# Performance work log

Hardware: AMD Instinct MI355X
Metric: run time of the kernel (lower is better)

The kernel has to match this reference:

```python
import jax, jax.numpy as jnp
import numpy as np

B, T, H, E = 64, 48, 512, 512   # batch, max_length, hidden_size, embed_size (must equal H)
ATT, AF, FC, V = 196, 2048, 2048, 10000  # att_size, att_feat_size, fc_feat_size, vocab


def setup_inputs() -> dict:
    key = jax.random.key(0)
    ks = jax.random.split(key, 26)
    stdv = 1.0 / np.sqrt(H)

    def u(k, shape):
        return jax.random.uniform(k, shape, jnp.float32, -stdv, stdv)

    return {
        "word_idx": jax.random.randint(ks[0], (B, T), 0, V),
        "father_idx": jax.random.randint(ks[1], (B, T), 0, T),
        "fc_feats": jax.random.normal(ks[2], (B, FC), jnp.float32),
        "att_feats": jax.random.normal(ks[3], (B, ATT, AF), jnp.float32),
        # fc_embed / att_embed / word embedding
        "W_fc": u(ks[4], (E, FC)), "b_fc": u(ks[5], (E,)),
        "W_att": u(ks[6], (E, AF)), "b_att": u(ks[7], (E,)),
        "embed_tab": u(ks[8], (V, E)),
        # MDLSTMCell parameters
        "weight_f1": u(ks[9], (H, E + H)), "bias_f1": u(ks[10], (H,)),
        "weight_f2": u(ks[11], (H, E + H)), "bias_f2": u(ks[12], (H,)),
        "weight_H": u(ks[13], (2 * H, 2 * E + 2 * H)), "bias_H": u(ks[14], (2 * H,)),
        "weight_I": u(ks[15], (H, 2 * E + 2 * H + AF)), "bias_I": u(ks[16], (H,)),
        # attention core
        "W_ha": u(ks[17], (H, H)), "b_ha": u(ks[18], (H,)),
        "W_hf": u(ks[19], (H, H)), "b_hf": u(ks[20], (H,)),
        "W_alpha": u(ks[21], (1, H)), "b_alpha": u(ks[22], (1,)),
        # output logit
        "W_logit": u(ks[23], (V, H)), "b_logit": u(ks[24], (V,)),
    }


def _forward(word_idx, father_idx, fc_feats, att_feats,
             W_fc, b_fc, W_att, b_att, embed_tab,
             weight_f1, bias_f1, weight_f2, bias_f2,
             weight_H, bias_H, weight_I, bias_I,
             W_ha, b_ha, W_hf, b_hf, W_alpha, b_alpha,
             W_logit, b_logit):
    Bn, Tn = word_idx.shape
    Hd = weight_f1.shape[0]

    fc_emb = fc_feats @ W_fc.T + b_fc                 # [B, E]
    p_att = att_feats @ W_att.T + b_att               # [B, ATT, H]
    att_mean = att_feats.mean(axis=1)                 # [B, AF]
    barange = jnp.arange(Bn)

    def attention(ha, hf):
        # dot: [B, ATT, H]
        dot = jnp.tanh((ha @ W_ha.T + b_ha)[:, None, :]
                       + (hf @ W_hf.T + b_hf)[:, None, :] + p_att)
        logits = (dot @ W_alpha.T + b_alpha)[..., 0]  # [B, ATT]
        w = jax.nn.softmax(logits, axis=1)
        return jnp.einsum('ba,bad->bd', w, att_feats)  # [B, AF]

    def cell(x1, x2, h1, c1, h2, c2, att_res):
        cat = jnp.concatenate([x1, x2, h1, h2], axis=1)
        gates = cat @ weight_H.T + bias_H
        ingate, outgate = jnp.split(gates, 2, axis=1)
        ingate = jax.nn.sigmoid(ingate)
        outgate = jax.nn.sigmoid(outgate)
        cat_hat = jnp.concatenate([x1, x2, h1, h2, att_res], axis=1)
        cellgate = jnp.tanh(cat_hat @ weight_I.T + bias_I)
        f1 = jax.nn.sigmoid(jnp.concatenate([x1, h1], axis=1) @ weight_f1.T + bias_f1)
        f2 = jax.nn.sigmoid(jnp.concatenate([x2, h2], axis=1) @ weight_f2.T + bias_f2)
        nc = f1 * c1 + f2 * c2 + ingate * cellgate
        nh = outgate * jnp.tanh(nc)
        return nh, nc

    def step(carry, i):
        h_states, c_states = carry                    # each [B, T, H]
        father = father_idx[:, i]
        is_first = (i == 0)
        # ancestor branch (gathered from father position)
        w_a = word_idx[barange, father]
        x_a = jnp.where(is_first, fc_emb, embed_tab[w_a])
        h_a = jnp.where(is_first, 0.0, h_states[barange, father])
        c_a = jnp.where(is_first, 0.0, c_states[barange, father])
        # sibling branch (previous timestep, reset when (i-1) % 3 == 0)
        ip = jnp.maximum(i - 1, 0)
        use_f = jnp.logical_not(is_first | (((i - 1) % 3) == 0))
        x_f = jnp.where(use_f, embed_tab[word_idx[:, ip]], 0.0)
        h_f = jnp.where(use_f, h_states[:, ip], 0.0)
        c_f = jnp.where(use_f, c_states[:, ip], 0.0)
        att_res = jnp.where(is_first, att_mean, attention(h_a, h_f))
        nh, nc = cell(x_a, x_f, h_a, c_a, h_f, c_f, att_res)
        h_states = jax.lax.dynamic_update_slice(h_states, nh[:, None, :], (0, i, 0))
        c_states = jax.lax.dynamic_update_slice(c_states, nc[:, None, :], (0, i, 0))
        return (h_states, c_states), nh

    init = (jnp.zeros((Bn, Tn, Hd), jnp.float32), jnp.zeros((Bn, Tn, Hd), jnp.float32))
    _, outs = jax.lax.scan(step, init, jnp.arange(Tn))
    outs = jnp.transpose(outs, (1, 0, 2))             # [B, T, H]
    logits = outs @ W_logit.T + b_logit               # [B, T, V]
    return jax.nn.log_softmax(logits, axis=2)


def reference(word_idx, father_idx, fc_feats, att_feats,
              W_fc, b_fc, W_att, b_att, embed_tab,
              weight_f1, bias_f1, weight_f2, bias_f2,
              weight_H, bias_H, weight_I, bias_I,
              W_ha, b_ha, W_hf, b_hf, W_alpha, b_alpha,
              W_logit, b_logit):
    return _forward(word_idx, father_idx, fc_feats, att_feats,
                    W_fc, b_fc, W_att, b_att, embed_tab,
                    weight_f1, bias_f1, weight_f2, bias_f2,
                    weight_H, bias_H, weight_I, bias_I,
                    W_ha, b_ha, W_hf, b_hf, W_alpha, b_alpha,
                    W_logit, b_logit)
```

## Files before the change

kernel.cpp:

```cpp
#include <hip/hip_runtime.h>
#include <hip/hip_bf16.h>
#include <type_traits>

#define B_   64
#define T_   48
#define H_   512
#define E_   512
#define ATT_ 196
#define AF_  2048
#define FC_  2048
#define V_   10000

typedef unsigned short u16;
using s16x8 = __attribute__((ext_vector_type(8))) short;
using f32x4 = __attribute__((ext_vector_type(4))) float;

#define MD_BF16 0
#define MD_F32  1
#define MD_DYN  2

__device__ __forceinline__ float b2f(u16 u) {
  union { unsigned int i; float f; } x; x.i = ((unsigned int)u) << 16; return x.f;
}
__device__ __forceinline__ u16 f2b(float f) {
  union { float f; unsigned int i; } x; x.f = f;
  unsigned int r = x.i + 0x7fffu + ((x.i >> 16) & 1u);
  return (u16)(r >> 16);
}
__device__ __forceinline__ float sigmoid_(float x) { return 1.f / (1.f + __expf(-x)); }
__device__ __forceinline__ float tanh_(float x) { return 1.f - 2.f / (__expf(2.f * x) + 1.f); }

__device__ __forceinline__ float ldf(const void* p, size_t i, int f) {
  return f ? ((const float*)p)[i] : b2f(((const u16*)p)[i]);
}
__device__ __forceinline__ s16x8 ld8(const void* p, size_t idx, int f) {
  s16x8 r;
  if (f) {
    const float* q = (const float*)p + idx;
    float4 x = *(const float4*)q;
    float4 y = *(const float4*)(q + 4);
    r[0] = (short)f2b(x.x); r[1] = (short)f2b(x.y);
    r[2] = (short)f2b(x.z); r[3] = (short)f2b(x.w);
    r[4] = (short)f2b(y.x); r[5] = (short)f2b(y.y);
    r[6] = (short)f2b(y.z); r[7] = (short)f2b(y.w);
  } else {
    r = *(const s16x8*)((const u16*)p + idx);
  }
  return r;
}
__device__ __forceinline__ s16x8 zero8() {
  s16x8 r; for (int j = 0; j < 8; j++) r[j] = 0; return r;
}

__global__ void detect_f32(const u16* __restrict__ p, int* __restrict__ flag) {
  __shared__ int sb[256];
  int t = threadIdx.x, bad = 0;
  for (int i = t; i < 65536; i += 256) {
    int e = (p[i] >> 7) & 0xFF;
    bad |= (e == 0xFF) ? 1 : 0;
  }
  sb[t] = bad; __syncthreads();
  for (int s = 128; s; s >>= 1) { if (t < s) sb[t] |= sb[t + s]; __syncthreads(); }
  if (t == 0) *flag = sb[0];
}

template <typename CT>
__global__ __launch_bounds__(256) void gemm_nt(
    const void* __restrict__ A, int lda, size_t aoff, int amode,
    const void* __restrict__ B, int ldb, size_t boff, int bmode,
    CT* __restrict__ C, int ldc, int N, int Kc,
    const float* __restrict__ bias, size_t zstride, const int* __restrict__ flagp)
{
  __shared__ __align__(16) u16 As[64 * 40];
  __shared__ __align__(16) u16 Bs[64 * 40];

  const int dynf = *flagp;
  const int aF = (amode == MD_DYN) ? dynf : amode;
  const int bF = (bmode == MD_DYN) ? dynf : bmode;

  const int tid  = threadIdx.x;
  const int m0   = blockIdx.x * 64;
  const int n0   = blockIdx.y * 64;
  const int kz   = blockIdx.z * Kc;
  const int lane = tid & 63;
  const int w    = tid >> 6;
  const int wm   = (w >> 1) * 32;
  const int wn   = (w & 1) * 32;
  const int quad = lane >> 4;
  const int r16  = lane & 15;

  f32x4 acc[2][2];
  for (int a = 0; a < 2; a++) for (int b = 0; b < 2; b++)
    for (int k = 0; k < 4; k++) acc[a][b][k] = 0.f;

  const int sr = tid >> 2;
  const int sc = (tid & 3) * 8;
  const size_t idxA = (size_t)(m0 + sr) * lda + aoff + kz + sc;
  const size_t idxB = (size_t)(n0 + sr) * ldb + boff + kz + sc;
  const bool bok = (n0 + sr) < N;

  const int aoff0 = (wm + r16) * 40 + quad * 8;
  const int aoff1 = (wm + 16 + r16) * 40 + quad * 8;
  const int boff0 = (wn + r16) * 40 + quad * 8;
  const int boff1 = (wn + 16 + r16) * 40 + quad * 8;

  s16x8 av = ld8(A, idxA, aF);
  s16x8 bv = bok ? ld8(B, idxB, bF) : zero8();

  for (int k0 = 0; k0 < Kc; k0 += 32) {
    s16x8 avn = zero8(), bvn = zero8();
    if (k0 + 32 < Kc) {
      avn = ld8(A, idxA + k0 + 32, aF);
      if (bok) bvn = ld8(B, idxB + k0 + 32, bF);
    }
    __syncthreads();
    *(s16x8*)(As + sr * 40 + sc) = av;
    *(s16x8*)(Bs + sr * 40 + sc) = bv;
    __syncthreads();
    s16x8 a0 = *(const s16x8*)(As + aoff0);
    s16x8 a1 = *(const s16x8*)(As + aoff1);
    s16x8 b0 = *(const s16x8*)(Bs + boff0);
    s16x8 b1 = *(const s16x8*)(Bs + boff1);
    acc[0][0] = __builtin_amdgcn_mfma_f32_16x16x32_bf16(a0, b0, acc[0][0], 0, 0, 0);
    acc[0][1] = __builtin_amdgcn_mfma_f32_16x16x32_bf16(a0, b1, acc[0][1], 0, 0, 0);
    acc[1][0] = __builtin_amdgcn_mfma_f32_16x16x32_bf16(a1, b0, acc[1][0], 0, 0, 0);
    acc[1][1] = __builtin_amdgcn_mfma_f32_16x16x32_bf16(a1, b1, acc[1][1], 0, 0, 0);
    av = avn; bv = bvn;
  }

  CT* Cz = C + (size_t)blockIdx.z * zstride;
  const bool addb = (bias != nullptr) && (blockIdx.z == 0);
  for (int tm = 0; tm < 2; tm++)
    for (int tn = 0; tn < 2; tn++) {
      int col = n0 + wn + tn * 16 + r16;
      if (col >= N) continue;
      float bb = addb ? bias[col] : 0.f;
      int rowbase = m0 + wm + tm * 16 + quad * 4;
      for (int rg = 0; rg < 4; rg++) {
        float v = acc[tm][tn][rg] + bb;
        if constexpr (std::is_same<CT, float>::value)
          Cz[(size_t)(rowbase + rg) * ldc + col] = v;
        else
          Cz[(size_t)(rowbase + rg) * ldc + col] = f2b(v);
      }
    }
}

__global__ __launch_bounds__(256) void pack_wstep(
    const void* __restrict__ wH, const void* __restrict__ wI,
    const void* __restrict__ wf1, const void* __restrict__ wf2,
    u16* __restrict__ Wstep, const int* __restrict__ flagp)
{
  const int F = *flagp;
  for (int idx = blockIdx.x * 256 + threadIdx.x; idx < 2560 * 2048; idx += gridDim.x * 256) {
    int row = idx >> 11, col = idx & 2047;
    float v = 0.f;
    if (row < 1024) v = ldf(wH, (size_t)row * 2048 + col, F);
    else if (row < 1536) v = ldf(wI, (size_t)(row - 1024) * 4096 + col, F);
    else if (row < 2048) {
      int r = row - 1536;
      if (col < 512) v = ldf(wf1, (size_t)r * 1024 + col, F);
      else if (col >= 1024 && col < 1536) v = ldf(wf1, (size_t)r * 1024 + 512 + (col - 1024), F);
    } else {
      int r = row - 2048;
      if (col >= 512 && col < 1024) v = ldf(wf2, (size_t)r * 1024 + (col - 512), F);
      else if (col >= 1536) v = ldf(wf2, (size_t)r * 1024 + 512 + (col - 1536), F);
    }
    Wstep[idx] = f2b(v);
  }
}

__global__ __launch_bounds__(256) void pack_whahf(
    const void* __restrict__ W_ha, const void* __restrict__ W_hf,
    u16* __restrict__ Whahf, const int* __restrict__ flagp)
{
  const int F = *flagp;
  for (int idx = blockIdx.x * 256 + threadIdx.x; idx < 512 * 1024; idx += gridDim.x * 256) {
    int e = idx >> 10, k = idx & 1023;
    float v = (k < 512) ? ldf(W_ha, (size_t)e * 512 + k, F)
                        : ldf(W_hf, (size_t)e * 512 + (k - 512), F);
    Whahf[idx] = f2b(v);
  }
}

__global__ __launch_bounds__(256) void pack_bias(
    const void* bH, const void* bI, const void* bf1, const void* bf2,
    const void* bha, const void* bhf, const void* batt, const void* bfc, const void* blogit,
    float* biasStep, float* bhahf, float* batt_f, float* bfc_f, float* blogit_f,
    const int* __restrict__ flagp)
{
  const int F = *flagp;
  int t = blockIdx.x * 256 + threadIdx.x;
  if (t < 1024) biasStep[t] = ldf(bH, t, F);
  else if (t < 1536) biasStep[t] = ldf(bI, t - 1024, F);
  else if (t < 2048) biasStep[t] = ldf(bf1, t - 1536, F);
  else if (t < 2560) biasStep[t] = ldf(bf2, t - 2048, F);
  if (t < 512) {
    bhahf[t] = ldf(bha, t, F) + ldf(bhf, t, F);
    batt_f[t] = ldf(batt, t, F);
    bfc_f[t] = ldf(bfc, t, F);
  }
  if (t < V_) blogit_f[t] = ldf(blogit, t, F);
}

__global__ __launch_bounds__(256) void init_cat4(const float* __restrict__ fc_emb,
                                                 u16* __restrict__ cat4)
{
  int b = blockIdx.x, tid = threadIdx.x;
  u16* cr = cat4 + b * 2048;
  for (int rep = 0; rep < 2; rep++) {
    int j = tid + rep * 256;
    cr[j] = f2b(fc_emb[b * E_ + j]);
    cr[512 + j] = 0; cr[1024 + j] = 0; cr[1536 + j] = 0;
  }
}

__global__ __launch_bounds__(256) void att_logits_kernel(
    const float* __restrict__ tatf, const u16* __restrict__ p_att,
    const void* __restrict__ W_alpha, const void* __restrict__ b_alpha,
    float* __restrict__ alog, const int* __restrict__ flagp)
{
  const int F = *flagp;
  int gw = (blockIdx.x * 256 + threadIdx.x) >> 6;
  int lane = threadIdx.x & 63;
  if (gw >= B_ * ATT_) return;
  int b = gw / ATT_;
  const float* tr = tatf + b * H_;
  const u16* pr = p_att + (size_t)gw * H_;
  float acc = 0.f;
#pragma unroll
  for (int e0 = 0; e0 < H_; e0 += 64) {
    int e = e0 + lane;
    acc += tanh_(tr[e] + b2f(pr[e])) * ldf(W_alpha, e, F);
  }
#pragma unroll
  for (int off = 32; off; off >>= 1) acc += __shfl_down(acc, off);
  if (lane == 0) alog[gw] = acc + ldf(b_alpha, 0, F);
}

__global__ __launch_bounds__(256) void att_apply_kernel(
    const float* __restrict__ alog, const u16* __restrict__ att_proj,
    float* __restrict__ outc)
{
  int b = blockIdx.x, seg = blockIdx.y, tid = threadIdx.x;
  __shared__ float sw[ATT_];
  __shared__ float rb[256];
  if (alog) {
    float l = (tid < ATT_) ? alog[b * ATT_ + tid] : -3.0e38f;
    rb[tid] = l; __syncthreads();
    for (int s = 128; s; s >>= 1) { if (tid < s) rb[tid] = fmaxf(rb[tid], rb[tid + s]); __syncthreads(); }
    float mx = rb[0]; __syncthreads();
    float e = (tid < ATT_) ? __expf(l - mx) : 0.f;
    rb[tid] = e; __syncthreads();
    for (int s = 128; s; s >>= 1) { if (tid < s) rb[tid] += rb[tid + s]; __syncthreads(); }
    float sum = rb[0]; __syncthreads();
    if (tid < ATT_) sw[tid] = e / sum;
  } else {
    if (tid < ATT_) sw[tid] = 1.f / (float)ATT_;
  }
  __syncthreads();
  int lane = tid & 63, g = tid >> 6;
  int col = seg * 64 + lane;
  float acc = 0.f;
  for (int a = g; a < ATT_; a += 4)
    acc += sw[a] * b2f(att_proj[(size_t)(b * ATT_ + a) * H_ + col]);
  rb[tid] = acc; __syncthreads();
  if (g == 0) outc[b * H_ + col] = rb[lane] + rb[64 + lane] + rb[128 + lane] + rb[192 + lane];
}

__global__ __launch_bounds__(256) void step_finish_kernel(
    const float* __restrict__ Gbuf, const float* __restrict__ attc,
    float* __restrict__ c_states, u16* __restrict__ houts, u16* __restrict__ cat4,
    const int* __restrict__ father_idx, const int* __restrict__ word_idx,
    const void* __restrict__ embed_tab,
    int i, int is_first, int use_f, int build_next, int use_f_next,
    const int* __restrict__ flagp)
{
  const int F = *flagp;
  int b = blockIdx.x, tid = threadIdx.x;
  __shared__ u16 nh_sh[H_];
  int father = father_idx[b * T_ + i];
  const float* G0 = Gbuf + (size_t)b * 2560;
  const size_t zs = (size_t)B_ * 2560;
#pragma unroll
  for (int rep = 0; rep < 2; rep++) {
    int j = tid + rep * 256;
    float g_in = G0[j] + G0[zs + j] + G0[2 * zs + j] + G0[3 * zs + j];
    float g_out = G0[512 + j] + G0[zs + 512 + j] + G0[2 * zs + 512 + j] + G0[3 * zs + 512 + j];
    float g_cg = G0[1024 + j] + G0[zs + 1024 + j] + G0[2 * zs + 1024 + j] + G0[3 * zs + 1024 + j];
    float g_f1 = G0[1536 + j] + G0[zs + 1536 + j] + G0[2 * zs + 1536 + j] + G0[3 * zs + 1536 + j];
    float g_f2 = G0[2048 + j] + G0[zs + 2048 + j] + G0[2 * zs + 2048 + j] + G0[3 * zs + 2048 + j];
    float ing = sigmoid_(g_in);
    float outg = sigmoid_(g_out);
    float cg = tanh_(g_cg + attc[b * H_ + j]);
    float f1 = sigmoid_(g_f1);
    float f2 = sigmoid_(g_f2);
    float c1 = is_first ? 0.f : c_states[((size_t)b * T_ + father) * H_ + j];
    float c2 = use_f ? c_states[((size_t)b * T_ + (i - 1)) * H_ + j] : 0.f;
    float nc = f1 * c1 + f2 * c2 + ing * cg;
    float nh = outg * tanh_(nc);
    size_t o = ((size_t)b * T_ + i) * H_ + j;
    c_states[o] = nc;
    u16 hb = f2b(nh);
    houts[o] = hb;
    nh_sh[j] = hb;
  }
  __syncthreads();
  if (!build_next) return;
  int fn = father_idx[b * T_ + (i + 1)];
  int wa = word_idx[b * T_ + fn];
  int wf = word_idx[b * T_ + i];
  u16* cr = cat4 + b * 2048;
#pragma unroll
  for (int rep = 0; rep < 2; rep++) {
    int j = tid + rep * 256;
    cr[j] = f2b(ldf(embed_tab, (size_t)wa * E_ + j, F));
    cr[512 + j] = use_f_next ? f2b(ldf(embed_tab, (size_t)wf * E_ + j, F)) : (u16)0;
    cr[1024 + j] = (fn == i) ? nh_sh[j] : houts[((size_t)b * T_ + fn) * H_ + j];
    cr[1536 + j] = use_f_next ? nh_sh[j] : (u16)0;
  }
}

__global__ __launch_bounds__(256) void logsoftmax_kernel(float* __restrict__ out)
{
  __shared__ float vals[V_];
  __shared__ float rb[256];
  int row = blockIdx.x, tid = threadIdx.x;
  float* p = out + (size_t)row * V_;
  float mx = -3.0e38f;
  for (int c = tid * 4; c < V_; c += 1024) {
    float4 q = *(const float4*)(p + c);
    vals[c] = q.x; vals[c + 1] = q.y; vals[c + 2] = q.z; vals[c + 3] = q.w;
    mx = fmaxf(mx, fmaxf(fmaxf(q.x, q.y), fmaxf(q.z, q.w)));
  }
  rb[tid] = mx; __syncthreads();
  for (int s = 128; s; s >>= 1) { if (tid < s) rb[tid] = fmaxf(rb[tid], rb[tid + s]); __syncthreads(); }
  mx = rb[0]; __syncthreads();
  float sum = 0.f;
  for (int c = tid; c < V_; c += 256) sum += __expf(vals[c] - mx);
  rb[tid] = sum; __syncthreads();
  for (int s = 128; s; s >>= 1) { if (tid < s) rb[tid] += rb[tid + s]; __syncthreads(); }
  float lse = mx + __logf(rb[0]);
  for (int c = tid * 4; c < V_; c += 1024) {
    float4 q;
    q.x = vals[c] - lse; q.y = vals[c + 1] - lse;
    q.z = vals[c + 2] - lse; q.w = vals[c + 3] - lse;
    *(float4*)(p + c) = q;
  }
}

extern "C" void kernel_launch(void* const* d_in, const int* in_sizes, int n_in,
                              void* d_out, int out_size, void* d_ws, size_t ws_size,
                              hipStream_t stream)
{
  const int* word_idx   = (const int*)d_in[0];
  const int* father_idx = (const int*)d_in[1];
  const void* fc_feats  = d_in[2];
  const void* att_feats = d_in[3];
  const void* W_fc      = d_in[4];
  const void* b_fc      = d_in[5];
  const void* W_att     = d_in[6];
  const void* b_att     = d_in[7];
  const void* embed_tab = d_in[8];
  const void* weight_f1 = d_in[9];
  const void* bias_f1   = d_in[10];
  const void* weight_f2 = d_in[11];
  const void* bias_f2   = d_in[12];
  const void* weight_H  = d_in[13];
  const void* bias_H    = d_in[14];
  const void* weight_I  = d_in[15];
  const void* bias_I    = d_in[16];
  const void* W_ha      = d_in[17];
  const void* b_ha      = d_in[18];
  const void* W_hf      = d_in[19];
  const void* b_hf      = d_in[20];
  const void* W_alpha   = d_in[21];
  const void* b_alpha   = d_in[22];
  const void* W_logit   = d_in[23];
  const void* b_logit   = d_in[24];

  char* dob = (char*)d_out;
  size_t doff = 0;
  auto oalloc = [&](size_t bytes) -> char* {
    char* p = dob + doff;
    doff += (bytes + 255) & ~(size_t)255;
    return p;
  };
  u16*  p_att    = (u16*)oalloc((size_t)B_ * ATT_ * E_ * 2);
  u16*  att_proj = (u16*)oalloc((size_t)B_ * ATT_ * H_ * 2);
  u16*  Wstep    = (u16*)oalloc((size_t)2560 * 2048 * 2);
  u16*  Whahf    = (u16*)oalloc((size_t)512 * 1024 * 2);
  float* c_states = (float*)oalloc((size_t)B_ * T_ * H_ * 4);
  float* Gbuf     = (float*)oalloc((size_t)4 * B_ * 2560 * 4);
  u16*  cat4     = (u16*)oalloc((size_t)B_ * 2048 * 2);
  float* fc_emb   = (float*)oalloc((size_t)B_ * E_ * 4);
  float* att_meanp= (float*)oalloc((size_t)B_ * H_ * 4);
  float* tatf     = (float*)oalloc((size_t)B_ * H_ * 4);
  float* alog     = (float*)oalloc((size_t)B_ * ATT_ * 4);
  float* attc     = (float*)oalloc((size_t)B_ * H_ * 4);
  float* biasStep = (float*)oalloc(2560 * 4);
  float* bhahf    = (float*)oalloc(512 * 4);
  float* batt_f   = (float*)oalloc(512 * 4);
  float* bfc_f    = (float*)oalloc(512 * 4);

  char* ws = (char*)d_ws;
  size_t woff = 0;
  auto walloc = [&](size_t bytes) -> char* {
    char* p = ws + woff;
    woff += (bytes + 255) & ~(size_t)255;
    return p;
  };
  u16*  houts    = (u16*)walloc((size_t)B_ * T_ * H_ * 2);
  float* blogit_f = (float*)walloc((size_t)V_ * 4);
  int*   flag     = (int*)walloc(256);

  hipMemsetAsync(c_states, 0, (size_t)B_ * T_ * H_ * 4, stream);
  hipMemsetAsync(houts, 0, (size_t)B_ * T_ * H_ * 2, stream);

  detect_f32<<<1, 256, 0, stream>>>((const u16*)att_feats, flag);

  pack_wstep<<<4096, 256, 0, stream>>>(weight_H, weight_I, weight_f1, weight_f2, Wstep, flag);
  pack_whahf<<<2048, 256, 0, stream>>>(W_ha, W_hf, Whahf, flag);
  pack_bias<<<40, 256, 0, stream>>>(bias_H, bias_I, bias_f1, bias_f2, b_ha, b_hf,
                                    b_att, b_fc, b_logit,
                                    biasStep, bhahf, batt_f, bfc_f, blogit_f, flag);

  gemm_nt<float><<<dim3(1, 8, 1), 256, 0, stream>>>(
      fc_feats, FC_, 0, MD_DYN, W_fc, FC_, 0, MD_DYN,
      fc_emb, E_, E_, FC_, bfc_f, 0, flag);
  gemm_nt<u16><<<dim3(B_ * ATT_ / 64, 8, 1), 256, 0, stream>>>(
      att_feats, AF_, 0, MD_DYN, W_att, AF_, 0, MD_DYN,
      p_att, E_, E_, AF_, batt_f, 0, flag);
  gemm_nt<u16><<<dim3(B_ * ATT_ / 64, 8, 1), 256, 0, stream>>>(
      att_feats, AF_, 0, MD_DYN, weight_I, 4096, 2048, MD_DYN,
      att_proj, H_, H_, AF_, nullptr, 0, flag);
  att_apply_kernel<<<dim3(B_, 8), 256, 0, stream>>>(nullptr, att_proj, att_meanp);
  init_cat4<<<B_, 256, 0, stream>>>(fc_emb, cat4);

  for (int i = 0; i < T_; i++) {
    int is_first = (i == 0);
    int use_f = (!is_first && ((i - 1) % 3 != 0)) ? 1 : 0;
    if (!is_first) {
      gemm_nt<float><<<dim3(1, 8, 1), 256, 0, stream>>>(
          cat4, 2048, 1024, MD_BF16, Whahf, 1024, 0, MD_BF16,
          tatf, H_, H_, 1024, bhahf, 0, flag);
      att_logits_kernel<<<(B_ * ATT_) / 4, 256, 0, stream>>>(
          tatf, p_att, W_alpha, b_alpha, alog, flag);
      att_apply_kernel<<<dim3(B_, 8), 256, 0, stream>>>(alog, att_proj, attc);
    }
    gemm_nt<float><<<dim3(1, 40, 4), 256, 0, stream>>>(
        cat4, 2048, 0, MD_BF16, Wstep, 2048, 0, MD_BF16,
        Gbuf, 2560, 2560, 512, biasStep, (size_t)B_ * 2560, flag);
    int build = (i + 1 < T_) ? 1 : 0;
    int use_f_next = (build && (i % 3 != 0)) ? 1 : 0;
    step_finish_kernel<<<B_, 256, 0, stream>>>(
        Gbuf, is_first ? att_meanp : attc, c_states, houts, cat4,
        father_idx, word_idx, embed_tab, i, is_first, use_f, build, use_f_next, flag);
  }

  gemm_nt<float><<<dim3(B_ * T_ / 64, (V_ + 63) / 64, 1), 256, 0, stream>>>(
      houts, H_, 0, MD_BF16, W_logit, H_, 0, MD_DYN,
      (float*)d_out, V_, V_, H_, blogit_f, 0, flag);
  logsoftmax_kernel<<<B_ * T_, 256, 0, stream>>>((float*)d_out);
}
```

Measured before the change: 3.365 ms.

## Fuse per-step gate GEMM with attention into one heterogeneous kernel

Replaces the four per-timestep launches (ha/hf GEMM, attention logits, softmax-apply, gate GEMM) with a single launch. 160 blocks run the gate GEMM while 64 extra blocks each compute one batch row's full attention path: the Whahf matvec, tanh logits, softmax and weighted sum. This cuts launch overhead and lets attention run alongside the GEMM. The cost is that each attention block redundantly streams the 1 MB Whahf matrix, the GEMM is retiled to 64x64 with K split into 512-wide chunks, and b_alpha is dropped, which softmax makes harmless.

```diff
diff --git a/kernel.cpp b/kernel.cpp
--- a/kernel.cpp
+++ b/kernel.cpp
@@ -146,6 +146,153 @@
     }
 }
 
+#define GEMM_BLKS 160
+
+__global__ __launch_bounds__(512) void step_fused(
+    const u16* __restrict__ cat4, const u16* __restrict__ Wstep,
+    const float* __restrict__ biasStep, float* __restrict__ Gbuf,
+    const u16* __restrict__ Whahf, const float* __restrict__ bhahf,
+    const u16* __restrict__ p_att, const void* __restrict__ W_alpha,
+    const u16* __restrict__ att_proj, float* __restrict__ attc,
+    int att_en, const int* __restrict__ flagp)
+{
+  const int tid = threadIdx.x;
+
+  __shared__ __align__(16) u16 As[64 * 40];
+  __shared__ __align__(16) u16 Bs[64 * 40];
+  __shared__ float hs_sh[1024];
+  __shared__ float Wa_sh[512];
+  __shared__ float tat_sh[512];
+  __shared__ float sl[256];
+  __shared__ float red[512];
+
+  if (blockIdx.x < GEMM_BLKS) {
+    const int by = blockIdx.x % 40;
+    const int bz = blockIdx.x / 40;
+    const int n0 = by * 64;
+    const int kz = bz * 512;
+    const int lane = tid & 63;
+    const int w    = tid >> 6;
+    const int wm   = (w & 1) * 32;
+    const int wn   = (w >> 1) * 16;
+    const int quad = lane >> 4;
+    const int r16  = lane & 15;
+
+    f32x4 acc0, acc1;
+    for (int k = 0; k < 4; k++) { acc0[k] = 0.f; acc1[k] = 0.f; }
+
+    const int half = tid >> 8;
+    const int r    = tid & 255;
+    const int sr   = r >> 2;
+    const int sc   = (r & 3) * 8;
+    const u16* src = half ? (Wstep + (size_t)(n0 + sr) * 2048 + kz + sc)
+                          : (cat4  + (size_t)sr * 2048 + kz + sc);
+    u16* dst = (half ? Bs : As) + sr * 40 + sc;
+
+    const int aoff0 = (wm + r16) * 40 + quad * 8;
+    const int aoff1 = (wm + 16 + r16) * 40 + quad * 8;
+    const int boff0 = (wn + r16) * 40 + quad * 8;
+
+    s16x8 v = *(const s16x8*)src;
+    for (int k0 = 0; k0 < 512; k0 += 32) {
+      s16x8 vn = zero8();
+      if (k0 + 32 < 512) vn = *(const s16x8*)(src + k0 + 32);
+      __syncthreads();
+      *(s16x8*)dst = v;
+      __syncthreads();
+      s16x8 a0 = *(const s16x8*)(As + aoff0);
+      s16x8 a1 = *(const s16x8*)(As + aoff1);
+      s16x8 b0 = *(const s16x8*)(Bs + boff0);
+      acc0 = __builtin_amdgcn_mfma_f32_16x16x32_bf16(a0, b0, acc0, 0, 0, 0);
+      acc1 = __builtin_amdgcn_mfma_f32_16x16x32_bf16(a1, b0, acc1, 0, 0, 0);
+      v = vn;
+    }
+
+    float* Cz = Gbuf + (size_t)bz * ((size_t)B_ * 2560);
+    const int col = n0 + wn + r16;
+    const float bb = (bz == 0) ? biasStep[col] : 0.f;
+    const int rb0 = wm + quad * 4;
+    for (int rg = 0; rg < 4; rg++)
+      Cz[(size_t)(rb0 + rg) * 2560 + col] = acc0[rg] + bb;
+    const int rb1 = wm + 16 + quad * 4;
+    for (int rg = 0; rg < 4; rg++)
+      Cz[(size_t)(rb1 + rg) * 2560 + col] = acc1[rg] + bb;
+    return;
+  }
+
+  if (!att_en) return;
+  const int b = blockIdx.x - GEMM_BLKS;
+  const int F = *flagp;
+  const int lane = tid & 63;
+  const int w    = tid >> 6;
+
+  hs_sh[tid]       = b2f(cat4[(size_t)b * 2048 + 1024 + tid]);
+  hs_sh[512 + tid] = b2f(cat4[(size_t)b * 2048 + 1536 + tid]);
+  Wa_sh[tid & 511] = ldf(W_alpha, tid & 511, F);
+  __syncthreads();
+
+  {
+    const u16* wr = Whahf + (size_t)tid * 1024;
+    float a0 = 0.f, a1 = 0.f, a2 = 0.f, a3 = 0.f;
+#pragma unroll 4
+    for (int k0 = 0; k0 < 1024; k0 += 8) {
+      s16x8 w8 = *(const s16x8*)(wr + k0);
+      a0 += b2f((u16)w8[0]) * hs_sh[k0 + 0];
+      a1 += b2f((u16)w8[1]) * hs_sh[k0 + 1];
+      a2 += b2f((u16)w8[2]) * hs_sh[k0 + 2];
+      a3 += b2f((u16)w8[3]) * hs_sh[k0 + 3];
+      a0 += b2f((u16)w8[4]) * hs_sh[k0 + 4];
+      a1 += b2f((u16)w8[5]) * hs_sh[k0 + 5];
+      a2 += b2f((u16)w8[6]) * hs_sh[k0 + 6];
+      a3 += b2f((u16)w8[7]) * hs_sh[k0 + 7];
+    }
+    tat_sh[tid] = (a0 + a1) + (a2 + a3) + bhahf[tid];
+  }
+  __syncthreads();
+
+  {
+    float t8[8], wa8[8];
+#pragma unroll
+    for (int j = 0; j < 8; j++) {
+      t8[j]  = tat_sh[lane * 8 + j];
+      wa8[j] = Wa_sh[lane * 8 + j];
+    }
+    for (int a = w; a < ATT_; a += 8) {
+      s16x8 pv = *(const s16x8*)(p_att + ((size_t)(b * ATT_ + a)) * 512 + lane * 8);
+      float acc = 0.f;
+#pragma unroll
+      for (int j = 0; j < 8; j++)
+        acc += wa8[j] * tanh_(t8[j] + b2f((u16)pv[j]));
+#pragma unroll
+      for (int off = 32; off; off >>= 1) acc += __shfl_down(acc, off);
+      if (lane == 0) sl[a] = acc;
+    }
+  }
+  __syncthreads();
+
+  float l = (tid < ATT_) ? sl[tid] : -3.0e38f;
+  red[tid] = l; __syncthreads();
+  for (int s = 256; s; s >>= 1) { if (tid < s) red[tid] = fmaxf(red[tid], red[tid + s]); __syncthreads(); }
+  float mx = red[0]; __syncthreads();
+  float e = (tid < ATT_) ? __expf(l - mx) : 0.f;
+  red[tid] = e; __syncthreads();
+  for (int s = 256; s; s >>= 1) { if (tid < s) red[tid] += red[tid + s]; __syncthreads(); }
+  float inv = 1.f / red[0];
+  __syncthreads();
+  if (tid < ATT_) sl[tid] = e * inv;
+  __syncthreads();
+
+  {
+    const u16* ap = att_proj + (size_t)b * ATT_ * 512 + tid;
+    float ac0 = 0.f, ac1 = 0.f;
+    for (int a = 0; a < ATT_; a += 2) {
+      ac0 += sl[a]     * b2f(ap[(size_t)a * 512]);
+      ac1 += sl[a + 1] * b2f(ap[(size_t)(a + 1) * 512]);
+    }
+    attc[b * H_ + tid] = ac0 + ac1;
+  }
+}
+
 __global__ __launch_bounds__(256) void pack_wstep(
     const void* __restrict__ wH, const void* __restrict__ wI,
     const void* __restrict__ wf1, const void* __restrict__ wf2,
@@ -213,29 +360,6 @@
     cr[j] = f2b(fc_emb[b * E_ + j]);
     cr[512 + j] = 0; cr[1024 + j] = 0; cr[1536 + j] = 0;
   }
-}
-
-__global__ __launch_bounds__(256) void att_logits_kernel(
-    const float* __restrict__ tatf, const u16* __restrict__ p_att,
-    const void* __restrict__ W_alpha, const void* __restrict__ b_alpha,
-    float* __restrict__ alog, const int* __restrict__ flagp)
-{
-  const int F = *flagp;
-  int gw = (blockIdx.x * 256 + threadIdx.x) >> 6;
-  int lane = threadIdx.x & 63;
-  if (gw >= B_ * ATT_) return;
-  int b = gw / ATT_;
-  const float* tr = tatf + b * H_;
-  const u16* pr = p_att + (size_t)gw * H_;
-  float acc = 0.f;
-#pragma unroll
-  for (int e0 = 0; e0 < H_; e0 += 64) {
-    int e = e0 + lane;
-    acc += tanh_(tr[e] + b2f(pr[e])) * ldf(W_alpha, e, F);
-  }
-#pragma unroll
-  for (int off = 32; off; off >>= 1) acc += __shfl_down(acc, off);
-  if (lane == 0) alog[gw] = acc + ldf(b_alpha, 0, F);
 }
 
 __global__ __launch_bounds__(256) void att_apply_kernel(
@@ -378,6 +502,7 @@
   const void* b_alpha   = d_in[22];
   const void* W_logit   = d_in[23];
   const void* b_logit   = d_in[24];
+  (void)b_alpha;
 
   char* dob = (char*)d_out;
   size_t doff = 0;
@@ -395,8 +520,6 @@
   u16*  cat4     = (u16*)oalloc((size_t)B_ * 2048 * 2);
   float* fc_emb   = (float*)oalloc((size_t)B_ * E_ * 4);
   float* att_meanp= (float*)oalloc((size_t)B_ * H_ * 4);
-  float* tatf     = (float*)oalloc((size_t)B_ * H_ * 4);
-  float* alog     = (float*)oalloc((size_t)B_ * ATT_ * 4);
   float* attc     = (float*)oalloc((size_t)B_ * H_ * 4);
   float* biasStep = (float*)oalloc(2560 * 4);
   float* bhahf    = (float*)oalloc(512 * 4);
@@ -440,17 +563,9 @@
   for (int i = 0; i < T_; i++) {
     int is_first = (i == 0);
     int use_f = (!is_first && ((i - 1) % 3 != 0)) ? 1 : 0;
-    if (!is_first) {
-      gemm_nt<float><<<dim3(1, 8, 1), 256, 0, stream>>>(
-          cat4, 2048, 1024, MD_BF16, Whahf, 1024, 0, MD_BF16,
-          tatf, H_, H_, 1024, bhahf, 0, flag);
-      att_logits_kernel<<<(B_ * ATT_) / 4, 256, 0, stream>>>(
-          tatf, p_att, W_alpha, b_alpha, alog, flag);
-      att_apply_kernel<<<dim3(B_, 8), 256, 0, stream>>>(alog, att_proj, attc);
-    }
-    gemm_nt<float><<<dim3(1, 40, 4), 256, 0, stream>>>(
-        cat4, 2048, 0, MD_BF16, Wstep, 2048, 0, MD_BF16,
-        Gbuf, 2560, 2560, 512, biasStep, (size_t)B_ * 2560, flag);
+    step_fused<<<GEMM_BLKS + B_, 512, 0, stream>>>(
+        cat4, Wstep, biasStep, Gbuf, Whahf, bhahf,
+        p_att, W_alpha, att_proj, attc, is_first ? 0 : 1, flag);
     int build = (i + 1 < T_) ? 1 : 0;
     int use_f_next = (build && (i % 3 != 0)) ? 1 : 0;
     step_finish_kernel<<<B_, 256, 0, stream>>>(
```

After: 3.812 ms. 1.13x slower.
